# Optimization experiments

Measured on AMD Instinct MI355X. Metric: run time of the kernel, lower is better.

Reference implementation:

```python
import jax, jax.numpy as jnp
import numpy as np

N_NODES = 100000


def _gcn_norm(edge_index, num_nodes):
    # add self loops
    src, dst = edge_index[0], edge_index[1]
    loop = jnp.arange(num_nodes, dtype=src.dtype)
    row = jnp.concatenate([src, loop])  # [E+N]
    col = jnp.concatenate([dst, loop])
    ew = jnp.ones(row.shape[0], dtype=jnp.float32)
    deg = jax.ops.segment_sum(ew, col, num_segments=num_nodes)  # [N]
    dinv = jnp.where(deg > 0, jax.lax.rsqrt(deg), 0.0)
    norm = dinv[row] * ew * dinv[col]  # [E+N]
    return row, col, norm


def setup_inputs() -> dict:
    key = jax.random.key(0)
    k1, k2, k3 = jax.random.split(key, 3)
    x = jax.random.normal(k1, (N_NODES, 64), dtype=jnp.float32)
    edge_index = jax.random.randint(k2, (2, 1280000), 0, N_NODES, dtype=jnp.int64)
    W = jax.random.normal(k3, (40, 64), dtype=jnp.float32) * (1.0 / np.sqrt(64))
    b = jnp.zeros((40,), dtype=jnp.float32)
    return {"x": x, "edge_index": edge_index, "W": W, "b": b}


def reference(x, edge_index, W, b):
    K = 3
    row, col, norm = _gcn_norm(edge_index, N_NODES)
    h = x
    for _ in range(K):
        # gather from source nodes, scale by symmetric norm, scatter-add to dst
        msg = norm[:, None] * h[row]  # [E+N, F]
        h = jax.ops.segment_sum(msg, col, num_segments=N_NODES)
    logits = h @ W.T + b  # [N, C]
    return jax.nn.log_softmax(logits, axis=1)
```

## Files before the change

kernel.cpp:

```cpp
#include <hip/hip_runtime.h>

#define F_IN 64
#define F_OUT 40
#define USTRIDE 20
#define QPN 5

#define PART_BLK 256
#define PART_EPB 16
#define PART_TILE (PART_BLK * PART_EPB)
#define BSHIFT 8
#define BCAP 4096
#define MAXB 512

#define WSTRIDE 17
#define NPB 51

__device__ inline unsigned pk2(float x, float y) {
    unsigned a = __float_as_uint(x); a = (a + 0x7FFFu + ((a >> 16) & 1u)) >> 16;
    unsigned b = __float_as_uint(y); b = (b + 0x7FFFu + ((b >> 16) & 1u)) >> 16;
    return a | (b << 16);
}
__device__ inline void up2(unsigned u, float& a, float& b) {
    a = __uint_as_float(u << 16); b = __uint_as_float(u & 0xFFFF0000u);
}

__global__ __launch_bounds__(PART_BLK) void partition_kernel(const int* __restrict__ src,
                                                             const int* __restrict__ dst,
                                                             int* __restrict__ bfill,
                                                             unsigned* __restrict__ staging,
                                                             int E, int nbk) {
    __shared__ int hist[MAXB];
    __shared__ int base[MAXB];
    int tid = threadIdx.x;
    for (int b = tid; b < nbk; b += PART_BLK) hist[b] = 0;
    __syncthreads();

    int rank[PART_EPB];
    int bk[PART_EPB];
    unsigned rec[PART_EPB];
    int eb = blockIdx.x * PART_TILE + tid;
#pragma unroll
    for (int k = 0; k < PART_EPB; ++k) {
        int e = eb + k * PART_BLK;
        if (e < E) {
            int r = src[e];
            int c = dst[e];
            int b = c >> BSHIFT;
            bk[k] = b;
            rec[k] = (unsigned)r | ((unsigned)(c & 255) << 17);
            rank[k] = atomicAdd(&hist[b], 1);
        } else {
            bk[k] = -1;
        }
    }
    __syncthreads();
    for (int b = tid; b < nbk; b += PART_BLK) {
        int h = hist[b];
        base[b] = h ? (b * BCAP + atomicAdd(&bfill[b], h)) : 0;
    }
    __syncthreads();
#pragma unroll
    for (int k = 0; k < PART_EPB; ++k) {
        if (bk[k] >= 0) staging[base[bk[k]] + rank[k]] = rec[k];
    }
}

__global__ __launch_bounds__(512) void btotal_scan_kernel(const int* __restrict__ bfill,
                                                          int* __restrict__ ebase,
                                                          int* __restrict__ rowptr_end,
                                                          int nbk, int E) {
    __shared__ int s[512];
    int tid = threadIdx.x;
    int v = (tid < nbk) ? bfill[tid] : 0;
    s[tid] = v;
    __syncthreads();
    for (int off = 1; off < 512; off <<= 1) {
        int t = (tid >= off) ? s[tid - off] : 0;
        __syncthreads();
        s[tid] += t;
        __syncthreads();
    }
    if (tid < nbk) ebase[tid] = s[tid] - v;
    if (tid == 0) *rowptr_end = E;
}

__global__ __launch_bounds__(256) void bucket_finalize_kernel(const unsigned* __restrict__ staging,
                                                              const int* __restrict__ bfill,
                                                              const int* __restrict__ ebase,
                                                              int* __restrict__ rowptr,
                                                              float* __restrict__ dinv,
                                                              float* __restrict__ dinv2,
                                                              int* __restrict__ srcs, int n) {
    int b = blockIdx.x;
    __shared__ int h[256];
    __shared__ int cur[256];
    int tid = threadIdx.x;
    h[tid] = 0;
    __syncthreads();

    int cnt = bfill[b];
    const unsigned* rec = staging + (size_t)b * BCAP;
    for (int i = tid; i < cnt; i += 256) {
        atomicAdd(&h[rec[i] >> 17], 1);
    }
    __syncthreads();

    int v = h[tid];
    for (int off = 1; off < 256; off <<= 1) {
        int t = (tid >= off) ? h[tid - off] : 0;
        __syncthreads();
        h[tid] += t;
        __syncthreads();
    }
    int excl = h[tid] - v;
    int base = ebase[b];
    int node = (b << BSHIFT) | tid;
    if (node < n) {
        rowptr[node] = base + excl;
        float r = rsqrtf((float)v + 1.0f);
        dinv[node] = r;
        dinv2[node] = r * r;
    }
    cur[tid] = base + excl;
    __syncthreads();

    for (int i = tid; i < cnt; i += 256) {
        unsigned rv = rec[i];
        int pos = atomicAdd(&cur[rv >> 17], 1);
        srcs[pos] = (int)(rv & 0x1FFFFu);
    }
}

__global__ __launch_bounds__(256, 4) void proj_kernel(const float* __restrict__ x,
                                                      const float* __restrict__ W,
                                                      const float* __restrict__ dinv,
                                                      unsigned* __restrict__ u, int n) {
    __shared__ float Ws[F_OUT * WSTRIDE * 4];
    for (int i = threadIdx.x; i < F_OUT * F_IN; i += 256) {
        int c = i >> 6;
        int k = i & 63;
        Ws[c * (WSTRIDE * 4) + k] = W[i];
    }
    __syncthreads();

    int t = blockIdx.x * 256 + threadIdx.x;
    int g = t >> 2;
    int q = t & 3;
    int n0 = 2 * g;
    if (n0 >= n) return;
    int n1 = n0 + 1;

    const float4* xp0 = (const float4*)(x + (size_t)n0 * F_IN);
    const float4* xp1 = (const float4*)(x + (size_t)n1 * F_IN);
    const float4* Wq  = (const float4*)Ws + (size_t)(q * 10) * WSTRIDE;

    float acc0[10], acc1[10];
#pragma unroll
    for (int c = 0; c < 10; ++c) { acc0[c] = 0.0f; acc1[c] = 0.0f; }

#pragma unroll 1
    for (int f4 = 0; f4 < F_IN / 4; ++f4) {
        float4 x0 = xp0[f4];
        float4 x1 = xp1[f4];
#pragma unroll
        for (int c = 0; c < 10; ++c) {
            float4 w = Wq[c * WSTRIDE + f4];
            acc0[c] += x0.x * w.x + x0.y * w.y + x0.z * w.z + x0.w * w.w;
            acc1[c] += x1.x * w.x + x1.y * w.y + x1.z * w.z + x1.w * w.w;
        }
    }

    float d0 = dinv[n0];
    float d1 = dinv[n1];
    unsigned* up0 = u + (size_t)n0 * USTRIDE + q * 5;
    unsigned* up1 = u + (size_t)n1 * USTRIDE + q * 5;
#pragma unroll
    for (int j = 0; j < 5; ++j) {
        up0[j] = pk2(d0 * acc0[2 * j], d0 * acc0[2 * j + 1]);
        up1[j] = pk2(d1 * acc1[2 * j], d1 * acc1[2 * j + 1]);
    }
}

__global__ __launch_bounds__(256) void propagate_kernel(const int* __restrict__ rowptr,
                                                        const int* __restrict__ srcs,
                                                        const float* __restrict__ dinv2,
                                                        const unsigned* __restrict__ ucur,
                                                        unsigned* __restrict__ unew, int n) {
    int t = blockIdx.x * blockDim.x + threadIdx.x;
    int node = t / QPN;
    int q = t - node * QPN;
    if (node >= n) return;

    int beg = rowptr[node];
    int end = rowptr[node + 1];

    const uint4* U = (const uint4*)ucur;
    uint4 sv = U[(size_t)node * QPN + q];
    float a0, a1, a2, a3, a4, a5, a6, a7;
    up2(sv.x, a0, a1); up2(sv.y, a2, a3); up2(sv.z, a4, a5); up2(sv.w, a6, a7);

    int i = beg;
    for (; i + 3 < end; i += 4) {
        int s0 = srcs[i], s1 = srcs[i + 1], s2 = srcs[i + 2], s3 = srcs[i + 3];
        uint4 v0 = U[(size_t)s0 * QPN + q];
        uint4 v1 = U[(size_t)s1 * QPN + q];
        uint4 v2 = U[(size_t)s2 * QPN + q];
        uint4 v3 = U[(size_t)s3 * QPN + q];
        float b0, b1;
        up2(v0.x, b0, b1); a0 += b0; a1 += b1;
        up2(v0.y, b0, b1); a2 += b0; a3 += b1;
        up2(v0.z, b0, b1); a4 += b0; a5 += b1;
        up2(v0.w, b0, b1); a6 += b0; a7 += b1;
        up2(v1.x, b0, b1); a0 += b0; a1 += b1;
        up2(v1.y, b0, b1); a2 += b0; a3 += b1;
        up2(v1.z, b0, b1); a4 += b0; a5 += b1;
        up2(v1.w, b0, b1); a6 += b0; a7 += b1;
        up2(v2.x, b0, b1); a0 += b0; a1 += b1;
        up2(v2.y, b0, b1); a2 += b0; a3 += b1;
        up2(v2.z, b0, b1); a4 += b0; a5 += b1;
        up2(v2.w, b0, b1); a6 += b0; a7 += b1;
        up2(v3.x, b0, b1); a0 += b0; a1 += b1;
        up2(v3.y, b0, b1); a2 += b0; a3 += b1;
        up2(v3.z, b0, b1); a4 += b0; a5 += b1;
        up2(v3.w, b0, b1); a6 += b0; a7 += b1;
    }
    for (; i < end; ++i) {
        uint4 v = U[(size_t)srcs[i] * QPN + q];
        float b0, b1;
        up2(v.x, b0, b1); a0 += b0; a1 += b1;
        up2(v.y, b0, b1); a2 += b0; a3 += b1;
        up2(v.z, b0, b1); a4 += b0; a5 += b1;
        up2(v.w, b0, b1); a6 += b0; a7 += b1;
    }

    float ds = dinv2[node];
    uint4 o;
    o.x = pk2(ds * a0, ds * a1);
    o.y = pk2(ds * a2, ds * a3);
    o.z = pk2(ds * a4, ds * a5);
    o.w = pk2(ds * a6, ds * a7);
    ((uint4*)unew)[(size_t)node * QPN + q] = o;
}

__global__ __launch_bounds__(256) void propagate_lsm_kernel(const int* __restrict__ rowptr,
                                                            const int* __restrict__ srcs,
                                                            const float* __restrict__ dinv,
                                                            const unsigned* __restrict__ ucur,
                                                            const float* __restrict__ bias,
                                                            float* __restrict__ out, int n) {
    __shared__ float red[256];
    int tid = threadIdx.x;
    int gl = tid / QPN;
    int q  = tid - gl * QPN;
    int node = blockIdx.x * NPB + gl;
    bool active = (gl < NPB) && (node < n);

    float a0 = 0, a1 = 0, a2 = 0, a3 = 0, a4 = 0, a5 = 0, a6 = 0, a7 = 0;
    float dv = 0.0f;
    if (active) {
        int beg = rowptr[node];
        int end = rowptr[node + 1];
        const uint4* U = (const uint4*)ucur;
        uint4 sv = U[(size_t)node * QPN + q];
        up2(sv.x, a0, a1); up2(sv.y, a2, a3); up2(sv.z, a4, a5); up2(sv.w, a6, a7);
        int i = beg;
        for (; i + 3 < end; i += 4) {
            int s0 = srcs[i], s1 = srcs[i + 1], s2 = srcs[i + 2], s3 = srcs[i + 3];
            uint4 v0 = U[(size_t)s0 * QPN + q];
            uint4 v1 = U[(size_t)s1 * QPN + q];
            uint4 v2 = U[(size_t)s2 * QPN + q];
            uint4 v3 = U[(size_t)s3 * QPN + q];
            float b0, b1;
            up2(v0.x, b0, b1); a0 += b0; a1 += b1;
            up2(v0.y, b0, b1); a2 += b0; a3 += b1;
            up2(v0.z, b0, b1); a4 += b0; a5 += b1;
            up2(v0.w, b0, b1); a6 += b0; a7 += b1;
            up2(v1.x, b0, b1); a0 += b0; a1 += b1;
            up2(v1.y, b0, b1); a2 += b0; a3 += b1;
            up2(v1.z, b0, b1); a4 += b0; a5 += b1;
            up2(v1.w, b0, b1); a6 += b0; a7 += b1;
            up2(v2.x, b0, b1); a0 += b0; a1 += b1;
            up2(v2.y, b0, b1); a2 += b0; a3 += b1;
            up2(v2.z, b0, b1); a4 += b0; a5 += b1;
            up2(v2.w, b0, b1); a6 += b0; a7 += b1;
            up2(v3.x, b0, b1); a0 += b0; a1 += b1;
            up2(v3.y, b0, b1); a2 += b0; a3 += b1;
            up2(v3.z, b0, b1); a4 += b0; a5 += b1;
            up2(v3.w, b0, b1); a6 += b0; a7 += b1;
        }
        for (; i < end; ++i) {
            uint4 v = U[(size_t)srcs[i] * QPN + q];
            float b0, b1;
            up2(v.x, b0, b1); a0 += b0; a1 += b1;
            up2(v.y, b0, b1); a2 += b0; a3 += b1;
            up2(v.z, b0, b1); a4 += b0; a5 += b1;
            up2(v.w, b0, b1); a6 += b0; a7 += b1;
        }
        dv = dinv[node];
    }

    float y0 = dv * a0 + bias[q * 8 + 0];
    float y1 = dv * a1 + bias[q * 8 + 1];
    float y2 = dv * a2 + bias[q * 8 + 2];
    float y3 = dv * a3 + bias[q * 8 + 3];
    float y4 = dv * a4 + bias[q * 8 + 4];
    float y5 = dv * a5 + bias[q * 8 + 5];
    float y6 = dv * a6 + bias[q * 8 + 6];
    float y7 = dv * a7 + bias[q * 8 + 7];

    float pm = fmaxf(fmaxf(fmaxf(y0, y1), fmaxf(y2, y3)),
                     fmaxf(fmaxf(y4, y5), fmaxf(y6, y7)));
    red[tid] = active ? pm : -1e30f;
    __syncthreads();
    int base = tid - q;
    float mx = fmaxf(fmaxf(fmaxf(red[base], red[base + 1]), fmaxf(red[base + 2], red[base + 3])),
                     red[base + 4]);
    __syncthreads();
    float ps = __expf(y0 - mx) + __expf(y1 - mx) + __expf(y2 - mx) + __expf(y3 - mx)
             + __expf(y4 - mx) + __expf(y5 - mx) + __expf(y6 - mx) + __expf(y7 - mx);
    red[tid] = active ? ps : 0.0f;
    __syncthreads();
    float se = red[base] + red[base + 1] + red[base + 2] + red[base + 3] + red[base + 4];
    float lse = mx + __logf(se);

    if (active) {
        float4* p = (float4*)(out + (size_t)node * F_OUT + q * 8);
        float4 o0, o1;
        o0.x = y0 - lse; o0.y = y1 - lse; o0.z = y2 - lse; o0.w = y3 - lse;
        o1.x = y4 - lse; o1.y = y5 - lse; o1.z = y6 - lse; o1.w = y7 - lse;
        p[0] = o0;
        p[1] = o1;
    }
}

extern "C" void kernel_launch(void* const* d_in, const int* in_sizes, int n_in,
                              void* d_out, int out_size, void* d_ws, size_t ws_size,
                              hipStream_t stream) {
    const float* x  = (const float*)d_in[0];
    const int*   ei = (const int*)d_in[1];
    const float* W  = (const float*)d_in[2];
    const float* b  = (const float*)d_in[3];

    const int N = in_sizes[0] / F_IN;
    const int E = in_sizes[1] / 2;
    const int* src = ei;
    const int* dst = ei + E;
    const int nbk = (N + (1 << BSHIFT) - 1) >> BSHIFT;

    char* base = (char*)d_ws;
    size_t off = 0;
    auto alloc = [&](size_t bytes) {
        char* p = base + off;
        off = (off + bytes + 255) & ~(size_t)255;
        return p;
    };
    float*    dinv    = (float*)   alloc((size_t)N * 4);
    float*    dinv2   = (float*)   alloc((size_t)N * 4);
    int*      rowptr  = (int*)     alloc((size_t)(N + 1) * 4);
    int*      bfill   = (int*)     alloc((size_t)MAXB * 4);
    int*      ebase   = (int*)     alloc((size_t)MAXB * 4);
    unsigned* staging = (unsigned*)alloc((size_t)nbk * BCAP * 4);
    int*      srcs_s  = (int*)     alloc((size_t)E * 4);
    unsigned* uA      = (unsigned*)alloc((size_t)N * USTRIDE * 4);
    unsigned* uB      = (unsigned*)alloc((size_t)N * USTRIDE * 4);
    float*    outp    = (float*)d_out;

    hipMemsetAsync(bfill, 0, (size_t)nbk * 4, stream);
    partition_kernel<<<(E + PART_TILE - 1) / PART_TILE, PART_BLK, 0, stream>>>(
        src, dst, bfill, staging, E, nbk);

    btotal_scan_kernel<<<1, 512, 0, stream>>>(bfill, ebase, rowptr + N, nbk, E);
    bucket_finalize_kernel<<<nbk, 256, 0, stream>>>(staging, bfill, ebase, rowptr,
                                                    dinv, dinv2, srcs_s, N);

    proj_kernel<<<((size_t)N * 2 + 255) / 256, 256, 0, stream>>>(x, W, dinv, uA, N);

    const int pt = N * QPN;
    const int pg = (pt + 255) / 256;
    propagate_kernel<<<pg, 256, 0, stream>>>(rowptr, srcs_s, dinv2, uA, uB, N);
    propagate_kernel<<<pg, 256, 0, stream>>>(rowptr, srcs_s, dinv2, uB, uA, N);

    const int fb = (N + NPB - 1) / NPB;
    propagate_lsm_kernel<<<fb, 256, 0, stream>>>(rowptr, srcs_s, dinv, uA, b, outp, N);
}
```

Baseline: 212.0 us.

## Relabel nodes by degree within each bucket to balance propagate work

Inside each 256-node bucket, nodes are bitonic-sorted by in-degree (descending) and given new labels. This adds origOf/sortOf maps, a remap pass over the edge source list, and indirect x reads and output writes. Neighbouring threads in propagate then get similar edge counts, which reduces wavefront divergence and load imbalance. The cost is an in-block sort, an extra full pass over the edges, and scattered gathers and stores at the graph boundaries.

Measured after the change: 229.5 us. 8.3% more time.

```diff
diff --git a/kernel.cpp b/kernel.cpp
--- a/kernel.cpp
+++ b/kernel.cpp
@@ -90,10 +90,15 @@
                                                               int* __restrict__ rowptr,
                                                               float* __restrict__ dinv,
                                                               float* __restrict__ dinv2,
-                                                              int* __restrict__ srcs, int n) {
+                                                              int* __restrict__ srcs,
+                                                              int* __restrict__ origOf,
+                                                              int* __restrict__ sortOf, int n) {
     int b = blockIdx.x;
     __shared__ int h[256];
+    __shared__ unsigned keys[256];
+    __shared__ int soff[256];
     __shared__ int cur[256];
+    __shared__ int slo[256];
     int tid = threadIdx.x;
     h[tid] = 0;
     __syncthreads();
@@ -105,24 +110,55 @@
     }
     __syncthreads();
 
-    int v = h[tid];
-    for (int off = 1; off < 256; off <<= 1) {
-        int t = (tid >= off) ? h[tid - off] : 0;
+    int deg = h[tid];
+    keys[tid] = ((unsigned)deg << 8) | (unsigned)(255 - tid);
+    __syncthreads();
+
+    for (int k = 2; k <= 256; k <<= 1) {
+        for (int j = k >> 1; j > 0; j >>= 1) {
+            int p = tid ^ j;
+            if (p > tid) {
+                unsigned a = keys[tid];
+                unsigned c = keys[p];
+                bool asc = ((tid & k) == 0);
+                if (asc ? (a < c) : (a > c)) {
+                    keys[tid] = c;
+                    keys[p] = a;
+                }
+            }
+            __syncthreads();
+        }
+    }
+
+    unsigned kk = keys[tid];
+    int o = 255 - (int)(kk & 255u);
+    int d = (int)(kk >> 8);
+
+    soff[tid] = d;
+    __syncthreads();
+    for (int off2 = 1; off2 < 256; off2 <<= 1) {
+        int t2 = (tid >= off2) ? soff[tid - off2] : 0;
         __syncthreads();
-        h[tid] += t;
+        soff[tid] += t2;
         __syncthreads();
     }
-    int excl = h[tid] - v;
+    int excl = soff[tid] - d;
     int base = ebase[b];
-    int node = (b << BSHIFT) | tid;
-    if (node < n) {
-        rowptr[node] = base + excl;
-        float r = rsqrtf((float)v + 1.0f);
-        dinv[node] = r;
-        dinv2[node] = r * r;
-    }
-    cur[tid] = base + excl;
-    __syncthreads();
+    int label = (b << BSHIFT) | tid;
+    int orig  = (b << BSHIFT) | o;
+    if (orig < n) {
+        rowptr[label] = base + excl;
+        float r = rsqrtf((float)d + 1.0f);
+        dinv[label] = r;
+        dinv2[label] = r * r;
+        origOf[label] = orig;
+    }
+    slo[o] = tid;
+    cur[o] = base + excl;
+    __syncthreads();
+
+    int mynode = (b << BSHIFT) | tid;
+    if (mynode < n) sortOf[mynode] = (b << BSHIFT) | slo[tid];
 
     for (int i = tid; i < cnt; i += 256) {
         unsigned rv = rec[i];
@@ -131,9 +167,22 @@
     }
 }
 
+__global__ void remap_kernel(int* __restrict__ srcs, const int* __restrict__ sortOf, int E) {
+    int i = (blockIdx.x * 256 + threadIdx.x) * 4;
+    if (i + 3 < E) {
+        int4 v = *(int4*)(srcs + i);
+        v.x = sortOf[v.x]; v.y = sortOf[v.y];
+        v.z = sortOf[v.z]; v.w = sortOf[v.w];
+        *(int4*)(srcs + i) = v;
+    } else {
+        for (; i < E; ++i) srcs[i] = sortOf[srcs[i]];
+    }
+}
+
 __global__ __launch_bounds__(256, 4) void proj_kernel(const float* __restrict__ x,
                                                       const float* __restrict__ W,
                                                       const float* __restrict__ dinv,
+                                                      const int* __restrict__ origOf,
                                                       unsigned* __restrict__ u, int n) {
     __shared__ float Ws[F_OUT * WSTRIDE * 4];
     for (int i = threadIdx.x; i < F_OUT * F_IN; i += 256) {
@@ -150,8 +199,10 @@
     if (n0 >= n) return;
     int n1 = n0 + 1;
 
-    const float4* xp0 = (const float4*)(x + (size_t)n0 * F_IN);
-    const float4* xp1 = (const float4*)(x + (size_t)n1 * F_IN);
+    int o0 = origOf[n0];
+    int o1 = origOf[n1];
+    const float4* xp0 = (const float4*)(x + (size_t)o0 * F_IN);
+    const float4* xp1 = (const float4*)(x + (size_t)o1 * F_IN);
     const float4* Wq  = (const float4*)Ws + (size_t)(q * 10) * WSTRIDE;
 
     float acc0[10], acc1[10];
@@ -245,6 +296,7 @@
 __global__ __launch_bounds__(256) void propagate_lsm_kernel(const int* __restrict__ rowptr,
                                                             const int* __restrict__ srcs,
                                                             const float* __restrict__ dinv,
+                                                            const int* __restrict__ origOf,
                                                             const unsigned* __restrict__ ucur,
                                                             const float* __restrict__ bias,
                                                             float* __restrict__ out, int n) {
@@ -324,7 +376,8 @@
     float lse = mx + __logf(se);
 
     if (active) {
-        float4* p = (float4*)(out + (size_t)node * F_OUT + q * 8);
+        int orig = origOf[node];
+        float4* p = (float4*)(out + (size_t)orig * F_OUT + q * 8);
         float4 o0, o1;
         o0.x = y0 - lse; o0.y = y1 - lse; o0.z = y2 - lse; o0.w = y3 - lse;
         o1.x = y4 - lse; o1.y = y5 - lse; o1.z = y6 - lse; o1.w = y7 - lse;
@@ -357,6 +410,8 @@
     float*    dinv    = (float*)   alloc((size_t)N * 4);
     float*    dinv2   = (float*)   alloc((size_t)N * 4);
     int*      rowptr  = (int*)     alloc((size_t)(N + 1) * 4);
+    int*      origOf  = (int*)     alloc((size_t)N * 4);
+    int*      sortOf  = (int*)     alloc((size_t)N * 4);
     int*      bfill   = (int*)     alloc((size_t)MAXB * 4);
     int*      ebase   = (int*)     alloc((size_t)MAXB * 4);
     unsigned* staging = (unsigned*)alloc((size_t)nbk * BCAP * 4);
@@ -371,9 +426,11 @@
 
     btotal_scan_kernel<<<1, 512, 0, stream>>>(bfill, ebase, rowptr + N, nbk, E);
     bucket_finalize_kernel<<<nbk, 256, 0, stream>>>(staging, bfill, ebase, rowptr,
-                                                    dinv, dinv2, srcs_s, N);
-
-    proj_kernel<<<((size_t)N * 2 + 255) / 256, 256, 0, stream>>>(x, W, dinv, uA, N);
+                                                    dinv, dinv2, srcs_s, origOf, sortOf, N);
+
+    remap_kernel<<<(E / 4 + 255) / 256 + 1, 256, 0, stream>>>(srcs_s, sortOf, E);
+
+    proj_kernel<<<((size_t)N * 2 + 255) / 256, 256, 0, stream>>>(x, W, dinv, origOf, uA, N);
 
     const int pt = N * QPN;
     const int pg = (pt + 255) / 256;
@@ -381,5 +438,5 @@
     propagate_kernel<<<pg, 256, 0, stream>>>(rowptr, srcs_s, dinv2, uB, uA, N);
 
     const int fb = (N + NPB - 1) / NPB;
-    propagate_lsm_kernel<<<fb, 256, 0, stream>>>(rowptr, srcs_s, dinv, uA, b, outp, N);
-}
+    propagate_lsm_kernel<<<fb, 256, 0, stream>>>(rowptr, srcs_s, dinv, origOf, uA, b, outp, N);
+}
```
